# Kernel tuning notes

Hardware: AMD Instinct MI355X
Metric: run time of the kernel (lower is better)

## Reference

```python
import jax, jax.numpy as jnp
import numpy as np

D_K = 64

def setup_inputs() -> dict:
    key = jax.random.key(0)
    k1, k2, k3, k4 = jax.random.split(key, 4)
    B, H, S, D = 2, 16, 2048, D_K
    Q = jax.random.normal(k1, (B, H, S, D), dtype=jnp.float32)
    K = jax.random.normal(k2, (B, H, S, D), dtype=jnp.float32)
    V = jax.random.normal(k3, (B, H, S, D), dtype=jnp.float32)
    attn_mask = jax.random.randint(k4, (B, H, S, S), 0, 2).astype(jnp.bool_)
    return {"Q": Q, "K": K, "V": V, "attn_mask": attn_mask}

def reference(Q, K, V, attn_mask):
    # scores: [B, H, S, S]
    scale = 1.0 / np.sqrt(D_K).astype(np.float32)
    scores = jnp.einsum('bhqd,bhkd->bhqk', Q, K) * scale
    scores = jnp.where(attn_mask, jnp.float32(-1e9), scores)
    attn = jax.nn.softmax(scores, axis=-1)
    context = jnp.einsum('bhqk,bhkd->bhqd', attn, V)
    return (context, attn)
```

## Files before the change

### kernel.cpp

```cpp
#include <hip/hip_runtime.h>


#define S_LEN 2048
#define D_DIM 64
#define NKT 32
#define QB 64

typedef __attribute__((ext_vector_type(8))) short bf16x8;
typedef __attribute__((ext_vector_type(4))) float f32x4;
typedef __attribute__((ext_vector_type(4))) unsigned short us4;

__device__ __forceinline__ unsigned short f2bf(float f) {
    unsigned u = __builtin_bit_cast(unsigned, f);
    u += 0x7fffu + ((u >> 16) & 1u);
    return (unsigned short)(u >> 16);
}
__device__ __forceinline__ float bf2f(unsigned short b) {
    return __builtin_bit_cast(float, (unsigned)b << 16);
}

typedef const __attribute__((address_space(1))) void cg_void;
typedef __attribute__((address_space(3))) void lds_void;
__device__ __forceinline__ void gload16(const void* g, void* l) {
    __builtin_amdgcn_global_load_lds((cg_void*)g, (lds_void*)l, 16, 0, 0);
}

__global__ __launch_bounds__(256)
void sdpa_prep(const float* __restrict__ K, const float* __restrict__ V,
               unsigned short* __restrict__ Kimg, unsigned short* __restrict__ Vimg)
{
    const int blk = blockIdx.x;
    const int bh = blk >> 5, kt = blk & 31;
    const float* Kt = K + ((size_t)bh * S_LEN + kt * 64) * D_DIM;
    const float* Vt = V + ((size_t)bh * S_LEN + kt * 64) * D_DIM;
    unsigned char* Kd = (unsigned char*)(Kimg + (size_t)blk * 4096);
    unsigned char* Vd = (unsigned char*)(Vimg + (size_t)blk * 4096);
    const int tid = threadIdx.x;

    {
        const int srow = tid >> 4, c4 = tid & 15;
        #pragma unroll
        for (int i = 0; i < 4; ++i) {
            int row = srow + i * 16;
            float4 v = *(const float4*)(Kt + (size_t)row * D_DIM + c4 * 4);
            us4 b = { f2bf(v.x), f2bf(v.y), f2bf(v.z), f2bf(v.w) };
            *(us4*)(Kd + row * 128 + (((c4 >> 1) ^ (row & 7)) << 4) + (c4 & 1) * 8) = b;
        }
    }
    {
        const int d = tid & 63, kg = tid >> 6;
        #pragma unroll
        for (int kk = 0; kk < 4; ++kk) {
            int k4 = kg * 4 + kk;
            int k0 = k4 * 4;
            float v0 = Vt[(size_t)(k0 + 0) * D_DIM + d];
            float v1 = Vt[(size_t)(k0 + 1) * D_DIM + d];
            float v2 = Vt[(size_t)(k0 + 2) * D_DIM + d];
            float v3 = Vt[(size_t)(k0 + 3) * D_DIM + d];
            us4 b = { f2bf(v0), f2bf(v1), f2bf(v2), f2bf(v3) };
            *(us4*)(Vd + d * 128 + (((k4 >> 1) ^ (d & 7)) << 4) + (k4 & 1) * 8) = b;
        }
    }
}

__global__ __launch_bounds__(256, 4)
void sdpa_main(const float* __restrict__ Q,
               const int* __restrict__ M,
               const unsigned short* __restrict__ Kimg,
               const unsigned short* __restrict__ Vimg,
               float* __restrict__ ctx_out,
               float* __restrict__ attn_out)
{
    __shared__ __align__(16) unsigned char smem[40960];
    unsigned short* const sK0 = (unsigned short*)(smem);
    unsigned short* const sK1 = (unsigned short*)(smem + 8192);
    unsigned short* const sV0 = (unsigned short*)(smem + 16384);
    unsigned short* const sV1 = (unsigned short*)(smem + 24576);
    unsigned short* const sPB = (unsigned short*)(smem + 32768);
    unsigned short* const sQl = (unsigned short*)(smem + 32768);

    const int tid  = threadIdx.x;
    const int lane = tid & 63;
    const int w    = tid >> 6;
    const int lq   = lane & 15;
    const int h    = lane >> 4;
    const int l7   = lq & 7;

    int b   = blockIdx.x;
    int swz = (b & 7) * 128 + (b >> 3);
    int bh  = swz >> 5, qt = swz & 31;
    const int q0 = qt * QB;

    const float* Qh = Q + ((size_t)bh * S_LEN + q0) * D_DIM;
    const int*   Mh = M + (size_t)bh * S_LEN * S_LEN;
    const unsigned short* Kh = Kimg + (size_t)bh * NKT * 4096;
    const unsigned short* Vh = Vimg + (size_t)bh * NKT * 4096;
    float* Ah = attn_out + (size_t)bh * S_LEN * S_LEN;
    float* Ch = ctx_out  + (size_t)bh * S_LEN * D_DIM;

    const int kf0 = ((h)     ^ l7) << 3;
    const int kf1 = ((4 + h) ^ l7) << 3;

    const int* Mb = Mh + (size_t)(q0 + w * 16 + h * 4) * S_LEN + lq;

    unsigned bits[4][4];
    #pragma unroll
    for (int jt = 0; jt < 4; ++jt)
        #pragma unroll
        for (int r = 0; r < 4; ++r)
            bits[jt][r] = 0u;

    #pragma unroll
    for (int tt = 0; tt < 2; ++tt)
        #pragma unroll
        for (int i = 0; i < 2; ++i)
            gload16((const unsigned char*)(Kh + (size_t)tt * 4096) + w * 2048 + i * 1024 + lane * 16,
                    smem + tt * 8192 + w * 2048 + i * 1024);
    __builtin_amdgcn_sched_barrier(0);

    #pragma unroll
    for (int tt = 0; tt < 2; ++tt)
        #pragma unroll
        for (int jt = 0; jt < 4; ++jt)
            #pragma unroll
            for (int r = 0; r < 4; ++r) {
                int m = Mb[(size_t)r * S_LEN + tt * 64 + jt * 16];
                bits[jt][r] |= (m ? 1u : 0u) << tt;
            }

    const float SC = 0.18033688011112042f;
    {
        const int srow = tid >> 4, c4 = tid & 15;
        #pragma unroll
        for (int i = 0; i < 4; ++i) {
            int row = srow + i * 16;
            float4 v = *(const float4*)(Qh + (size_t)row * D_DIM + c4 * 4);
            us4 bq = { f2bf(v.x * SC), f2bf(v.y * SC), f2bf(v.z * SC), f2bf(v.w * SC) };
            *(us4*)((unsigned char*)sQl + row * 128 + (((c4 >> 1) ^ (row & 7)) << 4) + (c4 & 1) * 8) = bq;
        }
    }
    __syncthreads();

    bf16x8 aq0 = *(const bf16x8*)(&sQl[(w * 16 + lq) * 64 + kf0]);
    bf16x8 aq1 = *(const bf16x8*)(&sQl[(w * 16 + lq) * 64 + kf1]);

    float lsum[4];
    #pragma unroll
    for (int r = 0; r < 4; ++r) lsum[r] = 0.f;

    for (int s = 0; s < 16; ++s) {
        const int kt0 = 2 * s;
        unsigned char* curp = smem + (s & 1) * 16384;
        unsigned char* nxtp = smem + ((s & 1) ^ 1) * 16384;
        const bool more = (s + 1 < 16);

        if (more) {
            #pragma unroll
            for (int tt = 0; tt < 2; ++tt)
                #pragma unroll
                for (int i = 0; i < 2; ++i)
                    gload16((const unsigned char*)(Kh + (size_t)(kt0 + 2 + tt) * 4096) + w * 2048 + i * 1024 + lane * 16,
                            nxtp + tt * 8192 + w * 2048 + i * 1024);
        }
        __builtin_amdgcn_sched_barrier(0);

        int mn[2][4][4];
        if (more) {
            #pragma unroll
            for (int tt = 0; tt < 2; ++tt)
                #pragma unroll
                for (int jt = 0; jt < 4; ++jt)
                    #pragma unroll
                    for (int r = 0; r < 4; ++r)
                        mn[tt][jt][r] = Mb[(size_t)r * S_LEN + (kt0 + 2 + tt) * 64 + jt * 16];
        }

        #pragma unroll
        for (int tt = 0; tt < 2; ++tt) {
            const unsigned short* kbuf = (const unsigned short*)(curp + tt * 8192);
            f32x4 acc[4];
            #pragma unroll
            for (int jt = 0; jt < 4; ++jt) {
                acc[jt] = (f32x4){0.f, 0.f, 0.f, 0.f};
                const unsigned short* kb = kbuf + (jt * 16 + lq) * 64;
                bf16x8 b0 = *(const bf16x8*)(kb + kf0);
                bf16x8 b1 = *(const bf16x8*)(kb + kf1);
                acc[jt] = __builtin_amdgcn_mfma_f32_16x16x32_bf16(aq0, b0, acc[jt], 0, 0, 0);
                acc[jt] = __builtin_amdgcn_mfma_f32_16x16x32_bf16(aq1, b1, acc[jt], 0, 0, 0);
            }
            #pragma unroll
            for (int r = 0; r < 4; ++r) {
                float e[4];
                #pragma unroll
                for (int jt = 0; jt < 4; ++jt) {
                    unsigned msk = (bits[jt][r] >> (kt0 + tt)) & 1u;
                    float ev = exp2f(acc[jt][r]);
                    e[jt] = msk ? 0.f : ev;
                }
                lsum[r] += (e[0] + e[1]) + (e[2] + e[3]);
            }
        }

        if (more) {
            #pragma unroll
            for (int tt = 0; tt < 2; ++tt)
                #pragma unroll
                for (int jt = 0; jt < 4; ++jt)
                    #pragma unroll
                    for (int r = 0; r < 4; ++r)
                        bits[jt][r] |= (mn[tt][jt][r] ? 1u : 0u) << (kt0 + 2 + tt);
        }
        __syncthreads();
    }

    float myIL[4];
    #pragma unroll
    for (int r = 0; r < 4; ++r) {
        float li = lsum[r];
        #pragma unroll
        for (int off = 1; off < 16; off <<= 1)
            li += __shfl_xor(li, off);
        myIL[r] = (li > 0.f) ? (1.f / li) : 0.f;
    }

    #pragma unroll
    for (int i = 0; i < 2; ++i) {
        gload16((const unsigned char*)Kh + w * 2048 + i * 1024 + lane * 16,
                (unsigned char*)sK0 + w * 2048 + i * 1024);
        gload16((const unsigned char*)Vh + w * 2048 + i * 1024 + lane * 16,
                (unsigned char*)sV0 + w * 2048 + i * 1024);
    }
    __syncthreads();

    f32x4 ctxa[4];
    #pragma unroll
    for (int dt = 0; dt < 4; ++dt) ctxa[dt] = (f32x4){0.f, 0.f, 0.f, 0.f};

    unsigned short* const sPw = sPB + w * 1024;
    float* const Abase = Ah + (size_t)(q0 + w * 16) * S_LEN;

    auto step2 = [&](unsigned short* curK, unsigned short* curV,
                     unsigned short* nxtK, unsigned short* nxtV, int kt) {
        const int ktn = (kt + 1 < NKT) ? kt + 1 : kt;
        #pragma unroll
        for (int i = 0; i < 2; ++i) {
            gload16((const unsigned char*)(Kh + (size_t)ktn * 4096) + w * 2048 + i * 1024 + lane * 16,
                    (unsigned char*)nxtK + w * 2048 + i * 1024);
            gload16((const unsigned char*)(Vh + (size_t)ktn * 4096) + w * 2048 + i * 1024 + lane * 16,
                    (unsigned char*)nxtV + w * 2048 + i * 1024);
        }
        __builtin_amdgcn_sched_barrier(0);

        f32x4 acc[4];
        #pragma unroll
        for (int jt = 0; jt < 4; ++jt) {
            acc[jt] = (f32x4){0.f, 0.f, 0.f, 0.f};
            const unsigned short* kb = curK + (jt * 16 + lq) * 64;
            bf16x8 b0 = *(const bf16x8*)(kb + kf0);
            bf16x8 b1 = *(const bf16x8*)(kb + kf1);
            acc[jt] = __builtin_amdgcn_mfma_f32_16x16x32_bf16(aq0, b0, acc[jt], 0, 0, 0);
            acc[jt] = __builtin_amdgcn_mfma_f32_16x16x32_bf16(aq1, b1, acc[jt], 0, 0, 0);
        }

        #pragma unroll
        for (int jt = 0; jt < 4; ++jt)
            #pragma unroll
            for (int r = 0; r < 4; ++r) {
                bool msk = (bits[jt][r] >> kt) & 1u;
                float p = exp2f(acc[jt][r]) * myIL[r];
                p = msk ? 0.f : p;
                int row = h * 4 + r;
                sPw[row * 64 + ((((jt << 1) | (lq >> 3)) ^ (row & 7)) << 3) + l7] = f2bf(p);
            }
        asm volatile("s_waitcnt lgkmcnt(0)" ::: "memory");
        __builtin_amdgcn_sched_barrier(0);

        float* Aw = Abase + kt * 64;
        #pragma unroll
        for (int it = 0; it < 4; ++it) {
            int row = it * 4 + h;
            us4 pb = *(const us4*)(&sPw[row * 64 + (((lq >> 1) ^ (row & 7)) << 3) + (lq & 1) * 4]);
            float4 pf = make_float4(bf2f(pb.x), bf2f(pb.y), bf2f(pb.z), bf2f(pb.w));
            *(float4*)(Aw + (size_t)row * S_LEN + lq * 4) = pf;
        }

        bf16x8 pa0 = *(const bf16x8*)(&sPw[lq * 64 + ((h ^ l7) << 3)]);
        bf16x8 pa1 = *(const bf16x8*)(&sPw[lq * 64 + (((4 + h) ^ l7) << 3)]);
        #pragma unroll
        for (int dt = 0; dt < 4; ++dt) {
            const unsigned short* vb = curV + (dt * 16 + lq) * 64;
            bf16x8 b0 = *(const bf16x8*)(vb + kf0);
            bf16x8 b1 = *(const bf16x8*)(vb + kf1);
            ctxa[dt] = __builtin_amdgcn_mfma_f32_16x16x32_bf16(pa0, b0, ctxa[dt], 0, 0, 0);
            ctxa[dt] = __builtin_amdgcn_mfma_f32_16x16x32_bf16(pa1, b1, ctxa[dt], 0, 0, 0);
        }
        __syncthreads();
    };

    for (int kt = 0; kt < NKT; kt += 2) {
        step2(sK0, sV0, sK1, sV1, kt);
        step2(sK1, sV1, sK0, sV0, kt + 1);
    }

    float* Crow = Ch + (size_t)(q0 + w * 16 + h * 4) * D_DIM;
    #pragma unroll
    for (int dt = 0; dt < 4; ++dt)
        #pragma unroll
        for (int r = 0; r < 4; ++r)
            Crow[(size_t)r * D_DIM + dt * 16 + lq] = ctxa[dt][r];
}

extern "C" void kernel_launch(void* const* d_in, const int* in_sizes, int n_in,
                              void* d_out, int out_size, void* d_ws, size_t ws_size,
                              hipStream_t stream)
{
    const float* Q = (const float*)d_in[0];
    const float* K = (const float*)d_in[1];
    const float* V = (const float*)d_in[2];
    const int*   M = (const int*)d_in[3];

    float* ctx  = (float*)d_out;
    float* attn = ctx + (size_t)2 * 16 * S_LEN * D_DIM;

    const size_t imgElems = (size_t)32 * NKT * 4096;
    if (ws_size < 2 * imgElems * sizeof(unsigned short)) return;
    unsigned short* Kimg = (unsigned short*)d_ws;
    unsigned short* Vimg = Kimg + imgElems;

    sdpa_prep<<<dim3(1024), 256, 0, stream>>>(K, V, Kimg, Vimg);
    sdpa_main<<<dim3(1024), 256, 0, stream>>>(Q, M, Kimg, Vimg, ctx, attn);
}
```

Measured before the change: 292.6 us.

## Read V fragments directly from global in MFMA order and stage two K tiles per barrier

The prep kernel now writes V in an MFMA-fragment-ordered layout, so each lane can load its B operand straight from global/L2 with one contiguous 16-byte load instead of going through LDS. The main loop now stages only K in LDS, double-buffering two K tiles per stage, which halves the number of block-wide barriers. This removes LDS traffic and sync cost for V. In exchange, the PV matmul sits directly on global-load latency, and each of the 4 waves rereads the same V data from cache.

```diff
diff --git a/kernel.cpp b/kernel.cpp
--- a/kernel.cpp
+++ b/kernel.cpp
@@ -33,9 +33,12 @@
     const int bh = blk >> 5, kt = blk & 31;
     const float* Kt = K + ((size_t)bh * S_LEN + kt * 64) * D_DIM;
     const float* Vt = V + ((size_t)bh * S_LEN + kt * 64) * D_DIM;
-    unsigned char* Kd = (unsigned char*)(Kimg + (size_t)blk * 4096);
-    unsigned char* Vd = (unsigned char*)(Vimg + (size_t)blk * 4096);
-    const int tid = threadIdx.x;
+    unsigned char*  Kd = (unsigned char*)(Kimg + (size_t)blk * 4096);
+    unsigned short* Vd = Vimg + (size_t)blk * 4096;
+    const int tid  = threadIdx.x;
+    const int lane = tid & 63;
+    const int lq   = lane & 15;
+    const int h    = lane >> 4;
 
     {
         const int srow = tid >> 4, c4 = tid & 15;
@@ -47,19 +50,17 @@
             *(us4*)(Kd + row * 128 + (((c4 >> 1) ^ (row & 7)) << 4) + (c4 & 1) * 8) = b;
         }
     }
-    {
-        const int d = tid & 63, kg = tid >> 6;
-        #pragma unroll
-        for (int kk = 0; kk < 4; ++kk) {
-            int k4 = kg * 4 + kk;
-            int k0 = k4 * 4;
-            float v0 = Vt[(size_t)(k0 + 0) * D_DIM + d];
-            float v1 = Vt[(size_t)(k0 + 1) * D_DIM + d];
-            float v2 = Vt[(size_t)(k0 + 2) * D_DIM + d];
-            float v3 = Vt[(size_t)(k0 + 3) * D_DIM + d];
-            us4 b = { f2bf(v0), f2bf(v1), f2bf(v2), f2bf(v3) };
-            *(us4*)(Vd + d * 128 + (((k4 >> 1) ^ (d & 7)) << 4) + (k4 & 1) * 8) = b;
-        }
+    #pragma unroll
+    for (int it = 0; it < 2; ++it) {
+        const int jtc = (tid >> 6) + it * 4;
+        const int dt  = jtc >> 1, c = jtc & 1;
+        const float* vs = Vt + (size_t)(c * 32 + h * 8) * D_DIM + dt * 16 + lq;
+        us4 v0 = { f2bf(vs[0 * D_DIM]), f2bf(vs[1 * D_DIM]),
+                   f2bf(vs[2 * D_DIM]), f2bf(vs[3 * D_DIM]) };
+        us4 v1 = { f2bf(vs[4 * D_DIM]), f2bf(vs[5 * D_DIM]),
+                   f2bf(vs[6 * D_DIM]), f2bf(vs[7 * D_DIM]) };
+        *(us4*)(Vd + jtc * 512 + lane * 8)     = v0;
+        *(us4*)(Vd + jtc * 512 + lane * 8 + 4) = v1;
     }
 }
 
@@ -72,10 +73,6 @@
                float* __restrict__ attn_out)
 {
     __shared__ __align__(16) unsigned char smem[40960];
-    unsigned short* const sK0 = (unsigned short*)(smem);
-    unsigned short* const sK1 = (unsigned short*)(smem + 8192);
-    unsigned short* const sV0 = (unsigned short*)(smem + 16384);
-    unsigned short* const sV1 = (unsigned short*)(smem + 24576);
     unsigned short* const sPB = (unsigned short*)(smem + 32768);
     unsigned short* const sQl = (unsigned short*)(smem + 32768);
 
@@ -224,12 +221,11 @@
     }
 
     #pragma unroll
-    for (int i = 0; i < 2; ++i) {
-        gload16((const unsigned char*)Kh + w * 2048 + i * 1024 + lane * 16,
-                (unsigned char*)sK0 + w * 2048 + i * 1024);
-        gload16((const unsigned char*)Vh + w * 2048 + i * 1024 + lane * 16,
-                (unsigned char*)sV0 + w * 2048 + i * 1024);
-    }
+    for (int tt = 0; tt < 2; ++tt)
+        #pragma unroll
+        for (int i = 0; i < 2; ++i)
+            gload16((const unsigned char*)(Kh + (size_t)tt * 4096) + w * 2048 + i * 1024 + lane * 16,
+                    smem + tt * 8192 + w * 2048 + i * 1024);
     __syncthreads();
 
     f32x4 ctxa[4];
@@ -239,67 +235,74 @@
     unsigned short* const sPw = sPB + w * 1024;
     float* const Abase = Ah + (size_t)(q0 + w * 16) * S_LEN;
 
-    auto step2 = [&](unsigned short* curK, unsigned short* curV,
-                     unsigned short* nxtK, unsigned short* nxtV, int kt) {
-        const int ktn = (kt + 1 < NKT) ? kt + 1 : kt;
-        #pragma unroll
-        for (int i = 0; i < 2; ++i) {
-            gload16((const unsigned char*)(Kh + (size_t)ktn * 4096) + w * 2048 + i * 1024 + lane * 16,
-                    (unsigned char*)nxtK + w * 2048 + i * 1024);
-            gload16((const unsigned char*)(Vh + (size_t)ktn * 4096) + w * 2048 + i * 1024 + lane * 16,
-                    (unsigned char*)nxtV + w * 2048 + i * 1024);
+    for (int s = 0; s < 16; ++s) {
+        const int kt0 = 2 * s;
+        unsigned char* curp = smem + (s & 1) * 16384;
+        unsigned char* nxtp = smem + ((s & 1) ^ 1) * 16384;
+        const bool more = (s + 1 < 16);
+
+        if (more) {
+            #pragma unroll
+            for (int tt = 0; tt < 2; ++tt)
+                #pragma unroll
+                for (int i = 0; i < 2; ++i)
+                    gload16((const unsigned char*)(Kh + (size_t)(kt0 + 2 + tt) * 4096) + w * 2048 + i * 1024 + lane * 16,
+                            nxtp + tt * 8192 + w * 2048 + i * 1024);
         }
         __builtin_amdgcn_sched_barrier(0);
 
-        f32x4 acc[4];
-        #pragma unroll
-        for (int jt = 0; jt < 4; ++jt) {
-            acc[jt] = (f32x4){0.f, 0.f, 0.f, 0.f};
-            const unsigned short* kb = curK + (jt * 16 + lq) * 64;
-            bf16x8 b0 = *(const bf16x8*)(kb + kf0);
-            bf16x8 b1 = *(const bf16x8*)(kb + kf1);
-            acc[jt] = __builtin_amdgcn_mfma_f32_16x16x32_bf16(aq0, b0, acc[jt], 0, 0, 0);
-            acc[jt] = __builtin_amdgcn_mfma_f32_16x16x32_bf16(aq1, b1, acc[jt], 0, 0, 0);
-        }
-
-        #pragma unroll
-        for (int jt = 0; jt < 4; ++jt)
-            #pragma unroll
-            for (int r = 0; r < 4; ++r) {
-                bool msk = (bits[jt][r] >> kt) & 1u;
-                float p = exp2f(acc[jt][r]) * myIL[r];
-                p = msk ? 0.f : p;
-                int row = h * 4 + r;
-                sPw[row * 64 + ((((jt << 1) | (lq >> 3)) ^ (row & 7)) << 3) + l7] = f2bf(p);
-            }
-        asm volatile("s_waitcnt lgkmcnt(0)" ::: "memory");
-        __builtin_amdgcn_sched_barrier(0);
-
-        float* Aw = Abase + kt * 64;
-        #pragma unroll
-        for (int it = 0; it < 4; ++it) {
-            int row = it * 4 + h;
-            us4 pb = *(const us4*)(&sPw[row * 64 + (((lq >> 1) ^ (row & 7)) << 3) + (lq & 1) * 4]);
-            float4 pf = make_float4(bf2f(pb.x), bf2f(pb.y), bf2f(pb.z), bf2f(pb.w));
-            *(float4*)(Aw + (size_t)row * S_LEN + lq * 4) = pf;
-        }
-
-        bf16x8 pa0 = *(const bf16x8*)(&sPw[lq * 64 + ((h ^ l7) << 3)]);
-        bf16x8 pa1 = *(const bf16x8*)(&sPw[lq * 64 + (((4 + h) ^ l7) << 3)]);
-        #pragma unroll
-        for (int dt = 0; dt < 4; ++dt) {
-            const unsigned short* vb = curV + (dt * 16 + lq) * 64;
-            bf16x8 b0 = *(const bf16x8*)(vb + kf0);
-            bf16x8 b1 = *(const bf16x8*)(vb + kf1);
-            ctxa[dt] = __builtin_amdgcn_mfma_f32_16x16x32_bf16(pa0, b0, ctxa[dt], 0, 0, 0);
-            ctxa[dt] = __builtin_amdgcn_mfma_f32_16x16x32_bf16(pa1, b1, ctxa[dt], 0, 0, 0);
+        #pragma unroll
+        for (int tt = 0; tt < 2; ++tt) {
+            const int kt = kt0 + tt;
+            const unsigned short* kbuf = (const unsigned short*)(curp + tt * 8192);
+
+            f32x4 acc[4];
+            #pragma unroll
+            for (int jt = 0; jt < 4; ++jt) {
+                acc[jt] = (f32x4){0.f, 0.f, 0.f, 0.f};
+                const unsigned short* kb = kbuf + (jt * 16 + lq) * 64;
+                bf16x8 b0 = *(const bf16x8*)(kb + kf0);
+                bf16x8 b1 = *(const bf16x8*)(kb + kf1);
+                acc[jt] = __builtin_amdgcn_mfma_f32_16x16x32_bf16(aq0, b0, acc[jt], 0, 0, 0);
+                acc[jt] = __builtin_amdgcn_mfma_f32_16x16x32_bf16(aq1, b1, acc[jt], 0, 0, 0);
+            }
+
+            asm volatile("s_waitcnt lgkmcnt(0)" ::: "memory");
+
+            #pragma unroll
+            for (int jt = 0; jt < 4; ++jt)
+                #pragma unroll
+                for (int r = 0; r < 4; ++r) {
+                    bool msk = (bits[jt][r] >> kt) & 1u;
+                    float p = exp2f(acc[jt][r]) * myIL[r];
+                    p = msk ? 0.f : p;
+                    int row = h * 4 + r;
+                    sPw[row * 64 + ((((jt << 1) | (lq >> 3)) ^ (row & 7)) << 3) + l7] = f2bf(p);
+                }
+            asm volatile("s_waitcnt lgkmcnt(0)" ::: "memory");
+            __builtin_amdgcn_sched_barrier(0);
+
+            float* Aw = Abase + kt * 64;
+            #pragma unroll
+            for (int it = 0; it < 4; ++it) {
+                int row = it * 4 + h;
+                us4 pb = *(const us4*)(&sPw[row * 64 + (((lq >> 1) ^ (row & 7)) << 3) + (lq & 1) * 4]);
+                float4 pf = make_float4(bf2f(pb.x), bf2f(pb.y), bf2f(pb.z), bf2f(pb.w));
+                *(float4*)(Aw + (size_t)row * S_LEN + lq * 4) = pf;
+            }
+
+            bf16x8 pa0 = *(const bf16x8*)(&sPw[lq * 64 + ((h ^ l7) << 3)]);
+            bf16x8 pa1 = *(const bf16x8*)(&sPw[lq * 64 + (((4 + h) ^ l7) << 3)]);
+            const unsigned short* vb = Vh + (size_t)kt * 4096;
+            #pragma unroll
+            for (int dt = 0; dt < 4; ++dt) {
+                bf16x8 v0 = *(const bf16x8*)(vb + (dt * 2 + 0) * 512 + lane * 8);
+                bf16x8 v1 = *(const bf16x8*)(vb + (dt * 2 + 1) * 512 + lane * 8);
+                ctxa[dt] = __builtin_amdgcn_mfma_f32_16x16x32_bf16(pa0, v0, ctxa[dt], 0, 0, 0);
+                ctxa[dt] = __builtin_amdgcn_mfma_f32_16x16x32_bf16(pa1, v1, ctxa[dt], 0, 0, 0);
+            }
         }
         __syncthreads();
-    };
-
-    for (int kt = 0; kt < NKT; kt += 2) {
-        step2(sK0, sV0, sK1, sV1, kt);
-        step2(sK1, sV1, sK0, sV0, kt + 1);
     }
 
     float* Crow = Ch + (size_t)(q0 + w * 16 + h * 4) * D_DIM;
```

New measurement: 361.6 us. 1.24x slower.

## Double query tile to 128 rows with 512-thread blocks and two-tile K/V stages

Applied to the files above, without the earlier changes.

Each block now processes 128 query rows with 8 waves instead of 64 rows with 4, halving the grid so every K/V tile loaded into LDS serves twice as many queries. The second pass now stages two K/V tiles per sync rather than one, which halves the number of barriers. LDS use per block doubles to 80 KB, which limits how many blocks fit on a CU, and barriers now span 8 waves.

```diff
diff --git a/kernel.cpp b/kernel.cpp
--- a/kernel.cpp
+++ b/kernel.cpp
@@ -4,7 +4,7 @@
 #define S_LEN 2048
 #define D_DIM 64
 #define NKT 32
-#define QB 64
+#define QB 128
 
 typedef __attribute__((ext_vector_type(8))) short bf16x8;
 typedef __attribute__((ext_vector_type(4))) float f32x4;
@@ -63,7 +63,7 @@
     }
 }
 
-__global__ __launch_bounds__(256, 4)
+__global__ __launch_bounds__(512, 4)
 void sdpa_main(const float* __restrict__ Q,
                const int* __restrict__ M,
                const unsigned short* __restrict__ Kimg,
@@ -71,12 +71,8 @@
                float* __restrict__ ctx_out,
                float* __restrict__ attn_out)
 {
-    __shared__ __align__(16) unsigned char smem[40960];
-    unsigned short* const sK0 = (unsigned short*)(smem);
-    unsigned short* const sK1 = (unsigned short*)(smem + 8192);
-    unsigned short* const sV0 = (unsigned short*)(smem + 16384);
-    unsigned short* const sV1 = (unsigned short*)(smem + 24576);
-    unsigned short* const sPB = (unsigned short*)(smem + 32768);
+    __shared__ __align__(16) unsigned char smem[81920];
+    unsigned short* const sPB = (unsigned short*)(smem + 65536);
     unsigned short* const sQl = (unsigned short*)(smem + 32768);
 
     const int tid  = threadIdx.x;
@@ -87,8 +83,8 @@
     const int l7   = lq & 7;
 
     int b   = blockIdx.x;
-    int swz = (b & 7) * 128 + (b >> 3);
-    int bh  = swz >> 5, qt = swz & 31;
+    int swz = (b & 7) * 64 + (b >> 3);
+    int bh  = swz >> 4, qt = swz & 15;
     const int q0 = qt * QB;
 
     const float* Qh = Q + ((size_t)bh * S_LEN + q0) * D_DIM;
@@ -112,10 +108,8 @@
 
     #pragma unroll
     for (int tt = 0; tt < 2; ++tt)
-        #pragma unroll
-        for (int i = 0; i < 2; ++i)
-            gload16((const unsigned char*)(Kh + (size_t)tt * 4096) + w * 2048 + i * 1024 + lane * 16,
-                    smem + tt * 8192 + w * 2048 + i * 1024);
+        gload16((const unsigned char*)(Kh + (size_t)tt * 4096) + tid * 16,
+                smem + tt * 8192 + tid * 16);
     __builtin_amdgcn_sched_barrier(0);
 
     #pragma unroll
@@ -130,10 +124,10 @@
 
     const float SC = 0.18033688011112042f;
     {
-        const int srow = tid >> 4, c4 = tid & 15;
         #pragma unroll
         for (int i = 0; i < 4; ++i) {
-            int row = srow + i * 16;
+            int f4 = tid + i * 512;
+            int row = f4 >> 4, c4 = f4 & 15;
             float4 v = *(const float4*)(Qh + (size_t)row * D_DIM + c4 * 4);
             us4 bq = { f2bf(v.x * SC), f2bf(v.y * SC), f2bf(v.z * SC), f2bf(v.w * SC) };
             *(us4*)((unsigned char*)sQl + row * 128 + (((c4 >> 1) ^ (row & 7)) << 4) + (c4 & 1) * 8) = bq;
@@ -157,10 +151,8 @@
         if (more) {
             #pragma unroll
             for (int tt = 0; tt < 2; ++tt)
-                #pragma unroll
-                for (int i = 0; i < 2; ++i)
-                    gload16((const unsigned char*)(Kh + (size_t)(kt0 + 2 + tt) * 4096) + w * 2048 + i * 1024 + lane * 16,
-                            nxtp + tt * 8192 + w * 2048 + i * 1024);
+                gload16((const unsigned char*)(Kh + (size_t)(kt0 + 2 + tt) * 4096) + tid * 16,
+                        nxtp + tt * 8192 + tid * 16);
         }
         __builtin_amdgcn_sched_barrier(0);
 
@@ -224,11 +216,11 @@
     }
 
     #pragma unroll
-    for (int i = 0; i < 2; ++i) {
-        gload16((const unsigned char*)Kh + w * 2048 + i * 1024 + lane * 16,
-                (unsigned char*)sK0 + w * 2048 + i * 1024);
-        gload16((const unsigned char*)Vh + w * 2048 + i * 1024 + lane * 16,
-                (unsigned char*)sV0 + w * 2048 + i * 1024);
+    for (int tt = 0; tt < 2; ++tt) {
+        gload16((const unsigned char*)(Kh + (size_t)tt * 4096) + tid * 16,
+                smem + tt * 8192 + tid * 16);
+        gload16((const unsigned char*)(Vh + (size_t)tt * 4096) + tid * 16,
+                smem + 32768 + tt * 8192 + tid * 16);
     }
     __syncthreads();
 
@@ -239,67 +231,78 @@
     unsigned short* const sPw = sPB + w * 1024;
     float* const Abase = Ah + (size_t)(q0 + w * 16) * S_LEN;
 
-    auto step2 = [&](unsigned short* curK, unsigned short* curV,
-                     unsigned short* nxtK, unsigned short* nxtV, int kt) {
-        const int ktn = (kt + 1 < NKT) ? kt + 1 : kt;
-        #pragma unroll
-        for (int i = 0; i < 2; ++i) {
-            gload16((const unsigned char*)(Kh + (size_t)ktn * 4096) + w * 2048 + i * 1024 + lane * 16,
-                    (unsigned char*)nxtK + w * 2048 + i * 1024);
-            gload16((const unsigned char*)(Vh + (size_t)ktn * 4096) + w * 2048 + i * 1024 + lane * 16,
-                    (unsigned char*)nxtV + w * 2048 + i * 1024);
+    for (int s = 0; s < 16; ++s) {
+        const int kt0 = 2 * s;
+        unsigned char* curK = smem + (s & 1) * 16384;
+        unsigned char* nxtK = smem + ((s & 1) ^ 1) * 16384;
+        unsigned char* curV = smem + 32768 + (s & 1) * 16384;
+        unsigned char* nxtV = smem + 32768 + ((s & 1) ^ 1) * 16384;
+        const bool more = (s + 1 < 16);
+
+        if (more) {
+            #pragma unroll
+            for (int tt = 0; tt < 2; ++tt) {
+                gload16((const unsigned char*)(Kh + (size_t)(kt0 + 2 + tt) * 4096) + tid * 16,
+                        nxtK + tt * 8192 + tid * 16);
+                gload16((const unsigned char*)(Vh + (size_t)(kt0 + 2 + tt) * 4096) + tid * 16,
+                        nxtV + tt * 8192 + tid * 16);
+            }
         }
         __builtin_amdgcn_sched_barrier(0);
 
-        f32x4 acc[4];
-        #pragma unroll
-        for (int jt = 0; jt < 4; ++jt) {
-            acc[jt] = (f32x4){0.f, 0.f, 0.f, 0.f};
-            const unsigned short* kb = curK + (jt * 16 + lq) * 64;
-            bf16x8 b0 = *(const bf16x8*)(kb + kf0);
-            bf16x8 b1 = *(const bf16x8*)(kb + kf1);
-            acc[jt] = __builtin_amdgcn_mfma_f32_16x16x32_bf16(aq0, b0, acc[jt], 0, 0, 0);
-            acc[jt] = __builtin_amdgcn_mfma_f32_16x16x32_bf16(aq1, b1, acc[jt], 0, 0, 0);
-        }
-
-        #pragma unroll
-        for (int jt = 0; jt < 4; ++jt)
-            #pragma unroll
-            for (int r = 0; r < 4; ++r) {
-                bool msk = (bits[jt][r] >> kt) & 1u;
-                float p = exp2f(acc[jt][r]) * myIL[r];
-                p = msk ? 0.f : p;
-                int row = h * 4 + r;
-                sPw[row * 64 + ((((jt << 1) | (lq >> 3)) ^ (row & 7)) << 3) + l7] = f2bf(p);
-            }
-        asm volatile("s_waitcnt lgkmcnt(0)" ::: "memory");
-        __builtin_amdgcn_sched_barrier(0);
-
-        float* Aw = Abase + kt * 64;
-        #pragma unroll
-        for (int it = 0; it < 4; ++it) {
-            int row = it * 4 + h;
-            us4 pb = *(const us4*)(&sPw[row * 64 + (((lq >> 1) ^ (row & 7)) << 3) + (lq & 1) * 4]);
-            float4 pf = make_float4(bf2f(pb.x), bf2f(pb.y), bf2f(pb.z), bf2f(pb.w));
-            *(float4*)(Aw + (size_t)row * S_LEN + lq * 4) = pf;
-        }
-
-        bf16x8 pa0 = *(const bf16x8*)(&sPw[lq * 64 + ((h ^ l7) << 3)]);
-        bf16x8 pa1 = *(const bf16x8*)(&sPw[lq * 64 + (((4 + h) ^ l7) << 3)]);
-        #pragma unroll
-        for (int dt = 0; dt < 4; ++dt) {
-            const unsigned short* vb = curV + (dt * 16 + lq) * 64;
-            bf16x8 b0 = *(const bf16x8*)(vb + kf0);
-            bf16x8 b1 = *(const bf16x8*)(vb + kf1);
-            ctxa[dt] = __builtin_amdgcn_mfma_f32_16x16x32_bf16(pa0, b0, ctxa[dt], 0, 0, 0);
-            ctxa[dt] = __builtin_amdgcn_mfma_f32_16x16x32_bf16(pa1, b1, ctxa[dt], 0, 0, 0);
+        #pragma unroll
+        for (int tt = 0; tt < 2; ++tt) {
+            const int kt = kt0 + tt;
+            const unsigned short* kbuf = (const unsigned short*)(curK + tt * 8192);
+
+            f32x4 acc[4];
+            #pragma unroll
+            for (int jt = 0; jt < 4; ++jt) {
+                acc[jt] = (f32x4){0.f, 0.f, 0.f, 0.f};
+                const unsigned short* kb = kbuf + (jt * 16 + lq) * 64;
+                bf16x8 b0 = *(const bf16x8*)(kb + kf0);
+                bf16x8 b1 = *(const bf16x8*)(kb + kf1);
+                acc[jt] = __builtin_amdgcn_mfma_f32_16x16x32_bf16(aq0, b0, acc[jt], 0, 0, 0);
+                acc[jt] = __builtin_amdgcn_mfma_f32_16x16x32_bf16(aq1, b1, acc[jt], 0, 0, 0);
+            }
+
+            asm volatile("s_waitcnt lgkmcnt(0)" ::: "memory");
+
+            #pragma unroll
+            for (int jt = 0; jt < 4; ++jt)
+                #pragma unroll
+                for (int r = 0; r < 4; ++r) {
+                    bool msk = (bits[jt][r] >> kt) & 1u;
+                    float p = exp2f(acc[jt][r]) * myIL[r];
+                    p = msk ? 0.f : p;
+                    int row = h * 4 + r;
+                    sPw[row * 64 + ((((jt << 1) | (lq >> 3)) ^ (row & 7)) << 3) + l7] = f2bf(p);
+                }
+            asm volatile("s_waitcnt lgkmcnt(0)" ::: "memory");
+            __builtin_amdgcn_sched_barrier(0);
+
+            float* Aw = Abase + kt * 64;
+            #pragma unroll
+            for (int it = 0; it < 4; ++it) {
+                int row = it * 4 + h;
+                us4 pb = *(const us4*)(&sPw[row * 64 + (((lq >> 1) ^ (row & 7)) << 3) + (lq & 1) * 4]);
+                float4 pf = make_float4(bf2f(pb.x), bf2f(pb.y), bf2f(pb.z), bf2f(pb.w));
+                *(float4*)(Aw + (size_t)row * S_LEN + lq * 4) = pf;
+            }
+
+            bf16x8 pa0 = *(const bf16x8*)(&sPw[lq * 64 + ((h ^ l7) << 3)]);
+            bf16x8 pa1 = *(const bf16x8*)(&sPw[lq * 64 + (((4 + h) ^ l7) << 3)]);
+            const unsigned short* vbuf = (const unsigned short*)(curV + tt * 8192);
+            #pragma unroll
+            for (int dt = 0; dt < 4; ++dt) {
+                const unsigned short* vb = vbuf + (dt * 16 + lq) * 64;
+                bf16x8 v0 = *(const bf16x8*)(vb + kf0);
+                bf16x8 v1 = *(const bf16x8*)(vb + kf1);
+                ctxa[dt] = __builtin_amdgcn_mfma_f32_16x16x32_bf16(pa0, v0, ctxa[dt], 0, 0, 0);
+                ctxa[dt] = __builtin_amdgcn_mfma_f32_16x16x32_bf16(pa1, v1, ctxa[dt], 0, 0, 0);
+            }
         }
         __syncthreads();
-    };
-
-    for (int kt = 0; kt < NKT; kt += 2) {
-        step2(sK0, sV0, sK1, sV1, kt);
-        step2(sK1, sV1, sK0, sV0, kt + 1);
     }
 
     float* Crow = Ch + (size_t)(q0 + w * 16 + h * 4) * D_DIM;
@@ -328,5 +331,5 @@
     unsigned short* Vimg = Kimg + imgElems;
 
     sdpa_prep<<<dim3(1024), 256, 0, stream>>>(K, V, Kimg, Vimg);
-    sdpa_main<<<dim3(1024), 256, 0, stream>>>(Q, M, Kimg, Vimg, ctx, attn);
-}
+    sdpa_main<<<dim3(512), 512, 0, stream>>>(Q, M, Kimg, Vimg, ctx, attn);
+}
```

Result: slower. 299.8 us (+2.4%).
